# Kernel tuning notes

Measured on AMD Instinct MI355X. Metric: run time of the kernel, lower is better.

The kernel has to match this reference:

```python
import jax, jax.numpy as jnp
import numpy as np
import math

B, C, H, W = 32, 256, 64, 64
AUX, RANK, HID, OS = 64, 64, 256, 8


def _fourier(u):
    # u: [B, r] -> take first r//2, sin/cos with freqs linspace(1, pi)
    half = RANK // 2
    w = jnp.linspace(1.0, math.pi, half, dtype=u.dtype)[None, :]
    u = u[:, :half]
    return jnp.concatenate([jnp.sin(u * w), jnp.cos(u * w)], axis=-1)


def setup_inputs() -> dict:
    key = jax.random.key(0)
    ks = jax.random.split(key, 10)

    def lin(k, fan_in, fan_out):
        k1, k2 = jax.random.split(k)
        Wm = jax.random.normal(k1, (fan_in, fan_out), jnp.float32) * 0.02
        bv = jax.random.normal(k2, (fan_out,), jnp.float32) * 0.02
        return Wm, bv

    d = C + AUX
    W_pre, b_pre = lin(ks[0], d, HID)
    W_bc, b_bc = lin(ks[1], HID, C)
    W_bs, b_bs = lin(ks[2], HID, OS)
    W_pc, b_pc = lin(ks[3], HID, RANK)
    W_ps, b_ps = lin(ks[4], HID, RANK)
    W_Wc, b_Wc = lin(ks[5], HID, C * RANK)
    W_Ws, b_Ws = lin(ks[6], HID, OS * RANK)
    x = jax.random.normal(ks[7], (B, C, H, W), jnp.float32)
    a = jax.random.normal(ks[8], (B, AUX), jnp.float32)
    return dict(x=x, a=a, W_pre=W_pre, b_pre=b_pre, W_bc=W_bc, b_bc=b_bc,
                W_bs=W_bs, b_bs=b_bs, W_pc=W_pc, b_pc=b_pc, W_ps=W_ps,
                b_ps=b_ps, W_Wc=W_Wc, b_Wc=b_Wc, W_Ws=W_Ws, b_Ws=b_Ws)


def _m2dm(x, a, W_pre, b_pre, W_bc, b_bc, W_bs, b_bs, W_pc, b_pc,
          W_ps, b_ps, W_Wc, b_Wc, W_Ws, b_Ws):
    Bn, Cn, Hn, Wn = x.shape
    # DynamicProjection
    g = x.mean(axis=(2, 3))                                    # [B,C] GAP
    h = jax.nn.relu(jnp.concatenate([g, a], axis=-1) @ W_pre + b_pre)
    m_base_c = h @ W_bc + b_bc                                 # [B,C]
    m_base_s = h @ W_bs + b_bs                                 # [B,8]
    phi_c = _fourier(h @ W_pc + b_pc)                          # [B,r]
    phi_s = _fourier(h @ W_ps + b_ps)                          # [B,r]
    Wc = (h @ W_Wc + b_Wc).reshape(Bn, Cn, RANK)
    Ws = (h @ W_Ws + b_Ws).reshape(Bn, OS, RANK)
    c_m = m_base_c * jnp.einsum('bcr,br->bc', Wc, phi_c)
    s_m = m_base_s * jnp.einsum('bsr,br->bs', Ws, phi_s)

    # channel modulation
    xc = x * jax.nn.sigmoid(c_m)[:, :, None, None]

    # SpatialModulation: per-sample cross-shaped 3x3 stencil on [avg,max]
    av = x.mean(axis=1)
    mx = x.max(axis=1)
    y = jnp.stack([av, mx], axis=1)                            # [B,2,H,W]
    p = s_m[:, :8].reshape(Bn, 2, 4)                           # up,down,left,right

    def shift(z, di, dj):
        # s[h,w] = z[h+di, w+dj] with zero padding (matches conv2d padding=1)
        zp = jnp.pad(z, ((0, 0), (0, 0), (1, 1), (1, 1)))
        return zp[:, :, 1 + di:1 + di + Hn, 1 + dj:1 + dj + Wn]

    up = shift(y, -1, 0)   # k[0,1] pairs with input row h-1
    dn = shift(y, 1, 0)    # k[2,1]
    lf = shift(y, 0, -1)   # k[1,0]
    rt = shift(y, 0, 1)    # k[1,2]
    pw = p[..., None, None]                                    # [B,2,4,1,1]
    center = -p.sum(axis=-1)[..., None, None]                  # k[1,1] = -sum
    conv = (pw[:, :, 0] * up + pw[:, :, 1] * dn +
            pw[:, :, 2] * lf + pw[:, :, 3] * rt + center * y).sum(axis=1)  # [B,H,W]
    xs = x * jax.nn.sigmoid(conv)[:, None, :, :]
    return x + xc + xs


def reference(x, a, W_pre, b_pre, W_bc, b_bc, W_bs, b_bs, W_pc, b_pc,
              W_ps, b_ps, W_Wc, b_Wc, W_Ws, b_Ws):
    return _m2dm(x, a, W_pre, b_pre, W_bc, b_bc, W_bs, b_bs, W_pc, b_pc,
                 W_ps, b_ps, W_Wc, b_Wc, W_Ws, b_Ws)
```

## Files before the change

kernel.cpp:

```cpp
#include <hip/hip_runtime.h>
#include <math.h>

#define BN   32
#define CN   256
#define HWN  4096
#define AUXN 64
#define RANKN 64
#define HIDN 256
#define OSN  8

#define WS_G    0
#define WS_H    8192
#define WS_PHIC 16384
#define WS_MBC  18432
#define WS_SM   26624
#define WS_SIGC 26880
#define WS_Y    35072
#define WS_SIGS 297216

__global__ __launch_bounds__(256) void k_gmean(const float* __restrict__ x,
                                               float* __restrict__ g) {
  int bc = blockIdx.x;
  const float4* xv = (const float4*)(x + (size_t)bc * HWN);
  int t = threadIdx.x;
  float s = 0.f;
#pragma unroll
  for (int i = 0; i < 4; i++) {
    float4 v = xv[t + 256 * i];
    s += v.x + v.y + v.z + v.w;
  }
  for (int off = 32; off; off >>= 1) s += __shfl_down(s, off, 64);
  __shared__ float wred[4];
  if ((t & 63) == 0) wred[t >> 6] = s;
  __syncthreads();
  if (t == 0) g[bc] = (wred[0] + wred[1] + wred[2] + wred[3]) * (1.0f / 4096.0f);
}

__global__ __launch_bounds__(256) void k_head(
    const float* __restrict__ g, const float* __restrict__ a,
    const float* __restrict__ W_pre, const float* __restrict__ b_pre,
    const float* __restrict__ W_bc,  const float* __restrict__ b_bc,
    const float* __restrict__ W_bs,  const float* __restrict__ b_bs,
    const float* __restrict__ W_pc,  const float* __restrict__ b_pc,
    const float* __restrict__ W_ps,  const float* __restrict__ b_ps,
    const float* __restrict__ W_Ws,  const float* __restrict__ b_Ws,
    float* __restrict__ h_out, float* __restrict__ phic_out,
    float* __restrict__ mbc_out, float* __restrict__ sm_out) {
  int b = blockIdx.x, t = threadIdx.x;
  __shared__ float in_s[320];
  __shared__ float h_s[256];
  __shared__ float phic_s[64], phis_s[64];
  __shared__ float red[512];
  in_s[t] = g[b * 256 + t];
  if (t < 64) in_s[256 + t] = a[b * 64 + t];
  __syncthreads();
  float acc = b_pre[t];
  for (int k = 0; k < 320; k++) acc = fmaf(in_s[k], W_pre[k * 256 + t], acc);
  float h = fmaxf(acc, 0.f);
  h_s[t] = h;
  h_out[b * 256 + t] = h;
  __syncthreads();
  if (t < 64) {
    int j = t & 31;
    const float* Wp = (t < 32) ? W_pc : W_ps;
    const float* bp = (t < 32) ? b_pc : b_ps;
    float u = bp[j];
    for (int k = 0; k < 256; k++) u = fmaf(h_s[k], Wp[k * 64 + j], u);
    float wj = 1.0f + (float)j * (3.14159265358979323846f - 1.0f) / 31.0f;
    float su = sinf(u * wj), cu = cosf(u * wj);
    float* ph = (t < 32) ? phic_s : phis_s;
    ph[j] = su;
    ph[32 + j] = cu;
  }
  __syncthreads();
  if (t < 64) phic_out[b * 64 + t] = phic_s[t];
  float mb = b_bc[t];
  for (int k = 0; k < 256; k++) mb = fmaf(h_s[k], W_bc[k * 256 + t], mb);
  mbc_out[b * 256 + t] = mb;
#pragma unroll
  for (int i = 0; i < 2; i++) {
    int idx = t + 256 * i;
    int s = idx >> 6, r = idx & 63;
    float v = b_Ws[s * 64 + r];
    for (int k = 0; k < 256; k++) v = fmaf(h_s[k], W_Ws[k * 512 + s * 64 + r], v);
    red[idx] = v * phis_s[r];
  }
  __syncthreads();
  if (t < 8) {
    float mbs = b_bs[t];
    for (int k = 0; k < 256; k++) mbs = fmaf(h_s[k], W_bs[k * 8 + t], mbs);
    float sum = 0.f;
    for (int r = 0; r < 64; r++) sum += red[t * 64 + r];
    sm_out[b * 8 + t] = mbs * sum;
  }
}

__global__ __launch_bounds__(512) void k_cm(
    const float* __restrict__ W_Wc, const float* __restrict__ b_Wc,
    const float* __restrict__ h_ws, const float* __restrict__ phic_ws,
    const float* __restrict__ mbc_ws, float* __restrict__ sigc_out) {
  int c = blockIdx.x, t = threadIdx.x;
  __shared__ __align__(16) float wsl[16384];
  __shared__ float h_s[256 * 32];
  __shared__ float phi_s[32 * 64];
  __shared__ float red[512];
  const float* col = W_Wc + (size_t)c * 64;
  for (int i = t; i < 16384; i += 512) {
    int k = i >> 6, r = i & 63;
    wsl[i] = col[(size_t)k * 16384 + r];
  }
  for (int i = t; i < 8192; i += 512) {
    int b = i >> 8, k = i & 255;
    h_s[k * 32 + b] = h_ws[i];
  }
  for (int i = t; i < 2048; i += 512) phi_s[i] = phic_ws[i];
  __syncthreads();
  int b = t >> 4, rq = t & 15;
  float4 q = {0.f, 0.f, 0.f, 0.f};
  const float4* wv = (const float4*)wsl;
  for (int k = 0; k < 256; k++) {
    float4 w4 = wv[k * 16 + rq];
    float hb = h_s[k * 32 + b];
    q.x = fmaf(hb, w4.x, q.x);
    q.y = fmaf(hb, w4.y, q.y);
    q.z = fmaf(hb, w4.z, q.z);
    q.w = fmaf(hb, w4.w, q.w);
  }
  int r0 = rq * 4;
  float4 bw = ((const float4*)(b_Wc + (size_t)c * 64))[rq];
  float part = (q.x + bw.x) * phi_s[b * 64 + r0 + 0] +
               (q.y + bw.y) * phi_s[b * 64 + r0 + 1] +
               (q.z + bw.z) * phi_s[b * 64 + r0 + 2] +
               (q.w + bw.w) * phi_s[b * 64 + r0 + 3];
  red[t] = part;
  __syncthreads();
  if (t < 32) {
    float sum = 0.f;
    for (int i = 0; i < 16; i++) sum += red[t * 16 + i];
    float v = mbc_ws[t * 256 + c] * sum;
    sigc_out[t * 256 + c] = 1.f / (1.f + expf(-v));
  }
}

__global__ __launch_bounds__(256) void k_avmx(const float* __restrict__ x,
                                              float* __restrict__ y) {
  int b = blockIdx.y;
  int px = blockIdx.x * 256 + threadIdx.x;
  const float* xb = x + (size_t)b * CN * HWN;
  float s = 0.f, m = -INFINITY;
#pragma unroll 8
  for (int c = 0; c < 256; c++) {
    float v = xb[(size_t)c * HWN + px];
    s += v;
    m = fmaxf(m, v);
  }
  y[(size_t)(b * 2 + 0) * HWN + px] = s * (1.0f / 256.0f);
  y[(size_t)(b * 2 + 1) * HWN + px] = m;
}

__global__ __launch_bounds__(256) void k_conv(const float* __restrict__ y,
                                              const float* __restrict__ sm,
                                              float* __restrict__ sigs) {
  int b = blockIdx.x, t = threadIdx.x;
  __shared__ float ys[2 * 4096];
  __shared__ float pc[10];
  for (int i = t; i < 8192; i += 256) ys[i] = y[b * 8192 + i];
  if (t < 8) pc[t] = sm[b * 8 + t];
  __syncthreads();
  if (t == 0) {
    pc[8] = -(pc[0] + pc[1] + pc[2] + pc[3]);
    pc[9] = -(pc[4] + pc[5] + pc[6] + pc[7]);
  }
  __syncthreads();
  for (int px = t; px < 4096; px += 256) {
    int i = px >> 6, j = px & 63;
    float conv = 0.f;
#pragma unroll
    for (int k = 0; k < 2; k++) {
      const float* yk = ys + k * 4096;
      float up = (i > 0)  ? yk[px - 64] : 0.f;
      float dn = (i < 63) ? yk[px + 64] : 0.f;
      float lf = (j > 0)  ? yk[px - 1]  : 0.f;
      float rt = (j < 63) ? yk[px + 1]  : 0.f;
      conv += pc[k * 4 + 0] * up + pc[k * 4 + 1] * dn + pc[k * 4 + 2] * lf +
              pc[k * 4 + 3] * rt + pc[8 + k] * yk[px];
    }
    sigs[b * 4096 + px] = 1.f / (1.f + expf(-conv));
  }
}

__global__ __launch_bounds__(256) void k_final(const float* __restrict__ x,
                                               const float* __restrict__ sigc,
                                               const float* __restrict__ sigs,
                                               float* __restrict__ out) {
  size_t idx4 = (size_t)blockIdx.x * 256 + threadIdx.x;
  size_t flat = idx4 * 4;
  int b = (int)(flat >> 20);
  int c = (int)((flat >> 12) & 255);
  int px = (int)(flat & 4095);
  float4 xv = ((const float4*)x)[idx4];
  float sc = 1.0f + sigc[b * 256 + c];
  float4 ss = ((const float4*)sigs)[((size_t)b * HWN + px) >> 2];
  float4 o;
  o.x = xv.x * (sc + ss.x);
  o.y = xv.y * (sc + ss.y);
  o.z = xv.z * (sc + ss.z);
  o.w = xv.w * (sc + ss.w);
  ((float4*)out)[idx4] = o;
}

extern "C" void kernel_launch(void* const* d_in, const int* in_sizes, int n_in,
                              void* d_out, int out_size, void* d_ws, size_t ws_size,
                              hipStream_t stream) {
  const float* x     = (const float*)d_in[0];
  const float* a     = (const float*)d_in[1];
  const float* W_pre = (const float*)d_in[2];
  const float* b_pre = (const float*)d_in[3];
  const float* W_bc  = (const float*)d_in[4];
  const float* b_bc  = (const float*)d_in[5];
  const float* W_bs  = (const float*)d_in[6];
  const float* b_bs  = (const float*)d_in[7];
  const float* W_pc  = (const float*)d_in[8];
  const float* b_pc  = (const float*)d_in[9];
  const float* W_ps  = (const float*)d_in[10];
  const float* b_ps  = (const float*)d_in[11];
  const float* W_Wc  = (const float*)d_in[12];
  const float* b_Wc  = (const float*)d_in[13];
  const float* W_Ws  = (const float*)d_in[14];
  const float* b_Ws  = (const float*)d_in[15];
  float* out = (float*)d_out;
  float* ws  = (float*)d_ws;

  float* g_ws    = ws + WS_G;
  float* h_ws    = ws + WS_H;
  float* phic_ws = ws + WS_PHIC;
  float* mbc_ws  = ws + WS_MBC;
  float* sm_ws   = ws + WS_SM;
  float* sigc_ws = ws + WS_SIGC;
  float* y_ws    = ws + WS_Y;
  float* sigs_ws = ws + WS_SIGS;

  k_gmean<<<BN * CN, 256, 0, stream>>>(x, g_ws);
  k_avmx<<<dim3(16, BN), 256, 0, stream>>>(x, y_ws);
  k_head<<<BN, 256, 0, stream>>>(g_ws, a, W_pre, b_pre, W_bc, b_bc, W_bs, b_bs,
                                 W_pc, b_pc, W_ps, b_ps, W_Ws, b_Ws,
                                 h_ws, phic_ws, mbc_ws, sm_ws);
  k_cm<<<CN, 512, 0, stream>>>(W_Wc, b_Wc, h_ws, phic_ws, mbc_ws, sigc_ws);
  k_conv<<<BN, 256, 0, stream>>>(y_ws, sm_ws, sigs_ws);
  k_final<<<(BN * CN * HWN) / 4 / 256, 256, 0, stream>>>(x, sigc_ws, sigs_ws, out);
}
```

Baseline: 389.3 us.

## Fuse channel-mean and avg/max stats into one pass; merge cm and conv kernels

The global-average-pool reduction is folded into the avg/max pass over x. Each block stages a 64-channel by 256-pixel tile in shared memory and writes per-tile partial channel sums, which the head kernel then adds up. This drops a second full read of x (about 128 MB). The channel-modulation and spatial-conv kernels are also merged into one launch with block-index dispatch, saving a launch and letting them run concurrently. The stats kernel gains heavy shared-memory use and extra syncs, and it launches only 512 blocks, which may limit occupancy and memory parallelism.

```diff
diff --git a/kernel.cpp b/kernel.cpp
--- a/kernel.cpp
+++ b/kernel.cpp
@@ -9,35 +9,57 @@
 #define HIDN 256
 #define OSN  8
 
-#define WS_G    0
-#define WS_H    8192
-#define WS_PHIC 16384
-#define WS_MBC  18432
-#define WS_SM   26624
-#define WS_SIGC 26880
-#define WS_Y    35072
-#define WS_SIGS 297216
-
-__global__ __launch_bounds__(256) void k_gmean(const float* __restrict__ x,
-                                               float* __restrict__ g) {
-  int bc = blockIdx.x;
-  const float4* xv = (const float4*)(x + (size_t)bc * HWN);
-  int t = threadIdx.x;
-  float s = 0.f;
-#pragma unroll
-  for (int i = 0; i < 4; i++) {
-    float4 v = xv[t + 256 * i];
-    s += v.x + v.y + v.z + v.w;
-  }
-  for (int off = 32; off; off >>= 1) s += __shfl_down(s, off, 64);
-  __shared__ float wred[4];
-  if ((t & 63) == 0) wred[t >> 6] = s;
-  __syncthreads();
-  if (t == 0) g[bc] = (wred[0] + wred[1] + wred[2] + wred[3]) * (1.0f / 4096.0f);
+#define WS_GPART 0
+#define WS_H     131072
+#define WS_PHIC  139264
+#define WS_MBC   141312
+#define WS_SM    149504
+#define WS_SIGC  149760
+#define WS_Y     157952
+#define WS_SIGS  420096
+
+#define TSTR 264
+
+__global__ __launch_bounds__(256) void k_stats(const float* __restrict__ x,
+                                               float* __restrict__ gpart,
+                                               float* __restrict__ y) {
+  int b = blockIdx.y, tile = blockIdx.x, t = threadIdx.x;
+  int px = tile * 256 + t;
+  const float* xb = x + (size_t)b * CN * HWN;
+  __shared__ __align__(16) float tl[64 * TSTR];
+  __shared__ float red[256];
+  float s = 0.f, m = -INFINITY;
+  float* gp = gpart + ((size_t)b * 16 + tile) * 256;
+  for (int cc = 0; cc < 4; cc++) {
+#pragma unroll 16
+    for (int cl = 0; cl < 64; cl++) {
+      float v = xb[(size_t)(cc * 64 + cl) * HWN + px];
+      s += v;
+      m = fmaxf(m, v);
+      tl[cl * TSTR + t] = v;
+    }
+    __syncthreads();
+    {
+      int cl = t >> 2, pg = t & 3;
+      const float4* row = (const float4*)(tl + cl * TSTR + pg * 64);
+      float4 acc = {0.f, 0.f, 0.f, 0.f};
+#pragma unroll
+      for (int j = 0; j < 16; j++) {
+        float4 v4 = row[j];
+        acc.x += v4.x; acc.y += v4.y; acc.z += v4.z; acc.w += v4.w;
+      }
+      red[t] = acc.x + acc.y + acc.z + acc.w;
+    }
+    __syncthreads();
+    if (t < 64) gp[cc * 64 + t] = red[t * 4] + red[t * 4 + 1] + red[t * 4 + 2] + red[t * 4 + 3];
+    __syncthreads();
+  }
+  y[(size_t)(b * 2 + 0) * HWN + px] = s * (1.0f / 256.0f);
+  y[(size_t)(b * 2 + 1) * HWN + px] = m;
 }
 
 __global__ __launch_bounds__(256) void k_head(
-    const float* __restrict__ g, const float* __restrict__ a,
+    const float* __restrict__ gpart, const float* __restrict__ a,
     const float* __restrict__ W_pre, const float* __restrict__ b_pre,
     const float* __restrict__ W_bc,  const float* __restrict__ b_bc,
     const float* __restrict__ W_bs,  const float* __restrict__ b_bs,
@@ -51,7 +73,12 @@
   __shared__ float h_s[256];
   __shared__ float phic_s[64], phis_s[64];
   __shared__ float red[512];
-  in_s[t] = g[b * 256 + t];
+  {
+    float gsum = 0.f;
+#pragma unroll
+    for (int tile = 0; tile < 16; tile++) gsum += gpart[((size_t)b * 16 + tile) * 256 + t];
+    in_s[t] = gsum * (1.0f / 4096.0f);
+  }
   if (t < 64) in_s[256 + t] = a[b * 64 + t];
   __syncthreads();
   float acc = b_pre[t];
@@ -95,97 +122,83 @@
   }
 }
 
-__global__ __launch_bounds__(512) void k_cm(
+__global__ __launch_bounds__(512) void k_cm_conv(
     const float* __restrict__ W_Wc, const float* __restrict__ b_Wc,
     const float* __restrict__ h_ws, const float* __restrict__ phic_ws,
-    const float* __restrict__ mbc_ws, float* __restrict__ sigc_out) {
-  int c = blockIdx.x, t = threadIdx.x;
-  __shared__ __align__(16) float wsl[16384];
-  __shared__ float h_s[256 * 32];
-  __shared__ float phi_s[32 * 64];
-  __shared__ float red[512];
-  const float* col = W_Wc + (size_t)c * 64;
-  for (int i = t; i < 16384; i += 512) {
-    int k = i >> 6, r = i & 63;
-    wsl[i] = col[(size_t)k * 16384 + r];
-  }
-  for (int i = t; i < 8192; i += 512) {
-    int b = i >> 8, k = i & 255;
-    h_s[k * 32 + b] = h_ws[i];
-  }
-  for (int i = t; i < 2048; i += 512) phi_s[i] = phic_ws[i];
-  __syncthreads();
-  int b = t >> 4, rq = t & 15;
-  float4 q = {0.f, 0.f, 0.f, 0.f};
-  const float4* wv = (const float4*)wsl;
-  for (int k = 0; k < 256; k++) {
-    float4 w4 = wv[k * 16 + rq];
-    float hb = h_s[k * 32 + b];
-    q.x = fmaf(hb, w4.x, q.x);
-    q.y = fmaf(hb, w4.y, q.y);
-    q.z = fmaf(hb, w4.z, q.z);
-    q.w = fmaf(hb, w4.w, q.w);
-  }
-  int r0 = rq * 4;
-  float4 bw = ((const float4*)(b_Wc + (size_t)c * 64))[rq];
-  float part = (q.x + bw.x) * phi_s[b * 64 + r0 + 0] +
-               (q.y + bw.y) * phi_s[b * 64 + r0 + 1] +
-               (q.z + bw.z) * phi_s[b * 64 + r0 + 2] +
-               (q.w + bw.w) * phi_s[b * 64 + r0 + 3];
-  red[t] = part;
-  __syncthreads();
-  if (t < 32) {
-    float sum = 0.f;
-    for (int i = 0; i < 16; i++) sum += red[t * 16 + i];
-    float v = mbc_ws[t * 256 + c] * sum;
-    sigc_out[t * 256 + c] = 1.f / (1.f + expf(-v));
-  }
-}
-
-__global__ __launch_bounds__(256) void k_avmx(const float* __restrict__ x,
-                                              float* __restrict__ y) {
-  int b = blockIdx.y;
-  int px = blockIdx.x * 256 + threadIdx.x;
-  const float* xb = x + (size_t)b * CN * HWN;
-  float s = 0.f, m = -INFINITY;
-#pragma unroll 8
-  for (int c = 0; c < 256; c++) {
-    float v = xb[(size_t)c * HWN + px];
-    s += v;
-    m = fmaxf(m, v);
-  }
-  y[(size_t)(b * 2 + 0) * HWN + px] = s * (1.0f / 256.0f);
-  y[(size_t)(b * 2 + 1) * HWN + px] = m;
-}
-
-__global__ __launch_bounds__(256) void k_conv(const float* __restrict__ y,
-                                              const float* __restrict__ sm,
-                                              float* __restrict__ sigs) {
-  int b = blockIdx.x, t = threadIdx.x;
-  __shared__ float ys[2 * 4096];
-  __shared__ float pc[10];
-  for (int i = t; i < 8192; i += 256) ys[i] = y[b * 8192 + i];
-  if (t < 8) pc[t] = sm[b * 8 + t];
-  __syncthreads();
-  if (t == 0) {
-    pc[8] = -(pc[0] + pc[1] + pc[2] + pc[3]);
-    pc[9] = -(pc[4] + pc[5] + pc[6] + pc[7]);
-  }
-  __syncthreads();
-  for (int px = t; px < 4096; px += 256) {
-    int i = px >> 6, j = px & 63;
-    float conv = 0.f;
-#pragma unroll
-    for (int k = 0; k < 2; k++) {
-      const float* yk = ys + k * 4096;
-      float up = (i > 0)  ? yk[px - 64] : 0.f;
-      float dn = (i < 63) ? yk[px + 64] : 0.f;
-      float lf = (j > 0)  ? yk[px - 1]  : 0.f;
-      float rt = (j < 63) ? yk[px + 1]  : 0.f;
-      conv += pc[k * 4 + 0] * up + pc[k * 4 + 1] * dn + pc[k * 4 + 2] * lf +
-              pc[k * 4 + 3] * rt + pc[8 + k] * yk[px];
-    }
-    sigs[b * 4096 + px] = 1.f / (1.f + expf(-conv));
+    const float* __restrict__ mbc_ws, float* __restrict__ sigc_out,
+    const float* __restrict__ y, const float* __restrict__ sm,
+    float* __restrict__ sigs) {
+  __shared__ __align__(16) float smem[27136];
+  int t = threadIdx.x;
+  if (blockIdx.x < 256) {
+    int c = blockIdx.x;
+    float* wsl   = smem;
+    float* h_s   = smem + 16384;
+    float* phi_s = smem + 24576;
+    float* red   = smem + 26624;
+    const float* col = W_Wc + (size_t)c * 64;
+    for (int i = t; i < 16384; i += 512) {
+      int k = i >> 6, r = i & 63;
+      wsl[i] = col[(size_t)k * 16384 + r];
+    }
+    for (int i = t; i < 8192; i += 512) {
+      int b = i >> 8, k = i & 255;
+      h_s[k * 32 + b] = h_ws[i];
+    }
+    for (int i = t; i < 2048; i += 512) phi_s[i] = phic_ws[i];
+    __syncthreads();
+    int b = t >> 4, rq = t & 15;
+    float4 q = {0.f, 0.f, 0.f, 0.f};
+    const float4* wv = (const float4*)wsl;
+    for (int k = 0; k < 256; k++) {
+      float4 w4 = wv[k * 16 + rq];
+      float hb = h_s[k * 32 + b];
+      q.x = fmaf(hb, w4.x, q.x);
+      q.y = fmaf(hb, w4.y, q.y);
+      q.z = fmaf(hb, w4.z, q.z);
+      q.w = fmaf(hb, w4.w, q.w);
+    }
+    int r0 = rq * 4;
+    float4 bw = ((const float4*)(b_Wc + (size_t)c * 64))[rq];
+    float part = (q.x + bw.x) * phi_s[b * 64 + r0 + 0] +
+                 (q.y + bw.y) * phi_s[b * 64 + r0 + 1] +
+                 (q.z + bw.z) * phi_s[b * 64 + r0 + 2] +
+                 (q.w + bw.w) * phi_s[b * 64 + r0 + 3];
+    red[t] = part;
+    __syncthreads();
+    if (t < 32) {
+      float sum = 0.f;
+      for (int i = 0; i < 16; i++) sum += red[t * 16 + i];
+      float v = mbc_ws[t * 256 + c] * sum;
+      sigc_out[t * 256 + c] = 1.f / (1.f + expf(-v));
+    }
+  } else {
+    int b = blockIdx.x - 256;
+    float* ys = smem;
+    float* pc = smem + 8192;
+    for (int i = t; i < 8192; i += 512) ys[i] = y[b * 8192 + i];
+    if (t < 8) pc[t] = sm[b * 8 + t];
+    __syncthreads();
+    if (t == 0) {
+      pc[8] = -(pc[0] + pc[1] + pc[2] + pc[3]);
+      pc[9] = -(pc[4] + pc[5] + pc[6] + pc[7]);
+    }
+    __syncthreads();
+    for (int px = t; px < 4096; px += 512) {
+      int i = px >> 6, j = px & 63;
+      float conv = 0.f;
+#pragma unroll
+      for (int k = 0; k < 2; k++) {
+        const float* yk = ys + k * 4096;
+        float up = (i > 0)  ? yk[px - 64] : 0.f;
+        float dn = (i < 63) ? yk[px + 64] : 0.f;
+        float lf = (j > 0)  ? yk[px - 1]  : 0.f;
+        float rt = (j < 63) ? yk[px + 1]  : 0.f;
+        conv += pc[k * 4 + 0] * up + pc[k * 4 + 1] * dn + pc[k * 4 + 2] * lf +
+                pc[k * 4 + 3] * rt + pc[8 + k] * yk[px];
+      }
+      sigs[b * 4096 + px] = 1.f / (1.f + expf(-conv));
+    }
   }
 }
 
@@ -231,21 +244,20 @@
   float* out = (float*)d_out;
   float* ws  = (float*)d_ws;
 
-  float* g_ws    = ws + WS_G;
-  float* h_ws    = ws + WS_H;
-  float* phic_ws = ws + WS_PHIC;
-  float* mbc_ws  = ws + WS_MBC;
-  float* sm_ws   = ws + WS_SM;
-  float* sigc_ws = ws + WS_SIGC;
-  float* y_ws    = ws + WS_Y;
-  float* sigs_ws = ws + WS_SIGS;
-
-  k_gmean<<<BN * CN, 256, 0, stream>>>(x, g_ws);
-  k_avmx<<<dim3(16, BN), 256, 0, stream>>>(x, y_ws);
-  k_head<<<BN, 256, 0, stream>>>(g_ws, a, W_pre, b_pre, W_bc, b_bc, W_bs, b_bs,
+  float* gpart_ws = ws + WS_GPART;
+  float* h_ws     = ws + WS_H;
+  float* phic_ws  = ws + WS_PHIC;
+  float* mbc_ws   = ws + WS_MBC;
+  float* sm_ws    = ws + WS_SM;
+  float* sigc_ws  = ws + WS_SIGC;
+  float* y_ws     = ws + WS_Y;
+  float* sigs_ws  = ws + WS_SIGS;
+
+  k_stats<<<dim3(16, BN), 256, 0, stream>>>(x, gpart_ws, y_ws);
+  k_head<<<BN, 256, 0, stream>>>(gpart_ws, a, W_pre, b_pre, W_bc, b_bc, W_bs, b_bs,
                                  W_pc, b_pc, W_ps, b_ps, W_Ws, b_Ws,
                                  h_ws, phic_ws, mbc_ws, sm_ws);
-  k_cm<<<CN, 512, 0, stream>>>(W_Wc, b_Wc, h_ws, phic_ws, mbc_ws, sigc_ws);
-  k_conv<<<BN, 256, 0, stream>>>(y_ws, sm_ws, sigs_ws);
+  k_cm_conv<<<CN + BN, 512, 0, stream>>>(W_Wc, b_Wc, h_ws, phic_ws, mbc_ws, sigc_ws,
+                                         y_ws, sm_ws, sigs_ws);
   k_final<<<(BN * CN * HWN) / 4 / 256, 256, 0, stream>>>(x, sigc_ws, sigs_ws, out);
 }
```

New measurement: 366.5 us. 5.9% less time.
